# Kernel optimization log

Hardware: AMD Instinct MI355X
Metric: run time of the kernel (lower is better)

## Reference

```python
import jax, jax.numpy as jnp
import numpy as np

N_NODES = 100000
N_EDGES = 1600000
IN_DIM = 128
OUT_DIM = 64
SLOPE = 0.2


def setup_inputs() -> dict:
    key = jax.random.key(0)
    k1, k2, k3, k4 = jax.random.split(key, 4)
    h = jax.random.normal(k1, (N_NODES, IN_DIM), dtype=jnp.float32)
    W = jax.random.normal(k2, (OUT_DIM, IN_DIM), dtype=jnp.float32) * (1.0 / np.sqrt(IN_DIM))
    src = jax.random.randint(k3, (N_EDGES,), 0, N_NODES, dtype=jnp.int64)
    dst = jax.random.randint(k4, (N_EDGES,), 0, N_NODES, dtype=jnp.int64)
    return {"h": h, "W": W, "src": src, "dst": dst}


def reference(h, W, src, dst):
    n = h.shape[0]
    z = h @ W.T                                   # [N, out_dim]
    z_src = z[src]                                # [E, out_dim]
    z_dst = z[dst]                                # [E, out_dim]
    e = jax.nn.leaky_relu(jnp.sum(z_src * z_dst, axis=1), negative_slope=SLOPE)  # [E]
    # segment softmax over incoming edges of each destination node
    m = jax.ops.segment_max(e, dst, num_segments=n)        # [N], -inf for isolated nodes
    ex = jnp.exp(e - m[dst])                                # [E]
    denom = jax.ops.segment_sum(ex, dst, num_segments=n)    # [N]
    alpha = ex / denom[dst]                                 # [E]
    agg = jax.ops.segment_sum(alpha[:, None] * z_src, dst, num_segments=n)  # [N, out_dim]
    return jax.nn.elu(agg)
```

## Files before the change

### kernel.cpp

```cpp
#include <hip/hip_runtime.h>
#include <math.h>

#define SLOPE 0.2f
#define LOG2E 1.4426950408889634f

__global__ __launch_bounds__(256) void gemm_hist_kernel(const float* __restrict__ h,
                                                        const float* __restrict__ W,
                                                        float* __restrict__ z,
                                                        const int* __restrict__ dst,
                                                        int* __restrict__ cnt,
                                                        int* __restrict__ rank,
                                                        int n, int ne) {
    int ei = blockIdx.x * 256 + threadIdx.x;
    int base = ei * 4;
    if (base + 3 < ne) {
        int4 d = *(const int4*)(dst + base);
        int4 r;
        r.x = atomicAdd(&cnt[d.x], 1);
        r.y = atomicAdd(&cnt[d.y], 1);
        r.z = atomicAdd(&cnt[d.z], 1);
        r.w = atomicAdd(&cnt[d.w], 1);
        *(int4*)(rank + base) = r;
    } else if (base < ne) {
        for (int rr = base; rr < ne; rr++) rank[rr] = atomicAdd(&cnt[dst[rr]], 1);
    }

    __shared__ float ws[128][68];
    int t = threadIdx.x;
    const float4* __restrict__ W4 = reinterpret_cast<const float4*>(W);
#pragma unroll
    for (int j = 0; j < 8; j++) {
        int idx = t + j * 256;
        float4 w = W4[idx];
        int o = idx >> 5;
        int k = (idx & 31) << 2;
        ws[k + 0][o] = w.x; ws[k + 1][o] = w.y;
        ws[k + 2][o] = w.z; ws[k + 3][o] = w.w;
    }
    __syncthreads();

    int nb = blockIdx.x * 64;
    int ng = t >> 4, og = t & 15;
    int n0 = nb + ng * 4;
    if (n0 >= n) return;
    const float* __restrict__ hp = h + (size_t)n0 * 128;

    float acc[4][4] = {};
#pragma unroll 4
    for (int k = 0; k < 128; k += 4) {
        float4 hv[4], wv[4];
#pragma unroll
        for (int i = 0; i < 4; i++) hv[i] = *(const float4*)(hp + i * 128 + k);
#pragma unroll
        for (int kk = 0; kk < 4; kk++) wv[kk] = *(const float4*)&ws[k + kk][og * 4];
#pragma unroll
        for (int i = 0; i < 4; i++) {
            acc[i][0] += hv[i].x * wv[0].x + hv[i].y * wv[1].x + hv[i].z * wv[2].x + hv[i].w * wv[3].x;
            acc[i][1] += hv[i].x * wv[0].y + hv[i].y * wv[1].y + hv[i].z * wv[2].y + hv[i].w * wv[3].y;
            acc[i][2] += hv[i].x * wv[0].z + hv[i].y * wv[1].z + hv[i].z * wv[2].z + hv[i].w * wv[3].z;
            acc[i][3] += hv[i].x * wv[0].w + hv[i].y * wv[1].w + hv[i].z * wv[2].w + hv[i].w * wv[3].w;
        }
    }
#pragma unroll
    for (int i = 0; i < 4; i++) {
        *(float4*)&z[(size_t)(n0 + i) * 64 + og * 4] =
            make_float4(acc[i][0], acc[i][1], acc[i][2], acc[i][3]);
    }
}

__global__ __launch_bounds__(256) void scan1(const int* __restrict__ cnt,
                                             int* __restrict__ starts,
                                             int* __restrict__ bsums, int n) {
    __shared__ int ls[256];
    int tbase = blockIdx.x * 4096 + threadIdx.x * 16;
    int v[16];
    int s = 0;
#pragma unroll
    for (int k = 0; k < 16; k++) {
        int idx = tbase + k;
        int c = idx < n ? cnt[idx] : 0;
        v[k] = c; s += c;
    }
    ls[threadIdx.x] = s;
    __syncthreads();
    for (int off = 1; off < 256; off <<= 1) {
        int t = threadIdx.x >= off ? ls[threadIdx.x - off] : 0;
        __syncthreads();
        ls[threadIdx.x] += t;
        __syncthreads();
    }
    int run = ls[threadIdx.x] - s;
    if (threadIdx.x == 255) bsums[blockIdx.x] = ls[255];
#pragma unroll
    for (int k = 0; k < 16; k++) {
        int idx = tbase + k;
        if (idx < n) starts[idx] = run;
        run += v[k];
    }
}

__global__ void scan2(int* __restrict__ bsums, int nb, int* __restrict__ starts,
                      int n, int ne) {
    if (threadIdx.x == 0) {
        int run = 0;
        for (int b = 0; b < nb; b++) { int t = bsums[b]; bsums[b] = run; run += t; }
        starts[n] = ne;
    }
}

__global__ __launch_bounds__(256) void scan3(int* __restrict__ starts,
                                             const int* __restrict__ bsums, int n) {
    int i = blockIdx.x * 256 + threadIdx.x;
    if (i < n) starts[i] += bsums[i >> 12];
}

__global__ __launch_bounds__(256) void scatter4_kernel(const int* __restrict__ src,
                                                       const int* __restrict__ dst,
                                                       const int* __restrict__ starts,
                                                       const int* __restrict__ rank,
                                                       int* __restrict__ csr_src, int ne) {
    int i = blockIdx.x * 256 + threadIdx.x;
    int base = i * 4;
    if (base + 3 < ne) {
        int4 s = *(const int4*)(src + base);
        int4 d = *(const int4*)(dst + base);
        int4 r = *(const int4*)(rank + base);
        csr_src[starts[d.x] + r.x] = s.x;
        csr_src[starts[d.y] + r.y] = s.y;
        csr_src[starts[d.z] + r.z] = s.z;
        csr_src[starts[d.w] + r.w] = s.w;
    } else {
        for (int r = base; r < ne; r++)
            csr_src[starts[dst[r]] + rank[r]] = src[r];
    }
}

__global__ __launch_bounds__(256) void fused_node(const float4* __restrict__ z4,
                                                  const int* __restrict__ starts,
                                                  const int* __restrict__ csr_src,
                                                  float4* __restrict__ out4, int n) {
    int node = blockIdx.x * 4 + (threadIdx.x >> 6);
    if (node >= n) return;
    int lane = threadIdx.x & 63;
    int g = lane >> 4;
    int q = lane & 15;
    int rs = starts[node], re = starts[node + 1];
    float4 zd = z4[(size_t)node * 16 + q];

    float m2 = -1e30f, denom = 0.f;
    float4 acc = make_float4(0.f, 0.f, 0.f, 0.f);

    for (int c = rs; c < re; c += 64) {
        int j = c + lane;
        int sv = j < re ? csr_src[j] : 0;
        int cn = min(64, re - c);
        int idx = g;
        bool val = idx < cn;
        int s = __shfl(sv, val ? idx : 0);
        float4 v = z4[(size_t)s * 16 + q];
        for (int k = 0; k < cn; k += 4) {
            int idx_n = k + 4 + g;
            bool val_n = idx_n < cn;
            int s_n = __shfl(sv, val_n ? idx_n : 0);
            float4 vn = z4[(size_t)s_n * 16 + q];
            float p = v.x * zd.x + v.y * zd.y + v.z * zd.z + v.w * zd.w;
#pragma unroll
            for (int msk = 1; msk < 16; msk <<= 1) p += __shfl_xor(p, msk);
            float e = p > 0.f ? p : SLOPE * p;
            float e2 = e * LOG2E;
            e2 = val ? e2 : -2e30f;
            if (__any(e2 > m2)) {
                float mnew = fmaxf(m2, e2);
                float sc = exp2f(m2 - mnew);
                float ex = exp2f(e2 - mnew);
                denom = fmaf(denom, sc, ex);
                acc.x = fmaf(acc.x, sc, ex * v.x);
                acc.y = fmaf(acc.y, sc, ex * v.y);
                acc.z = fmaf(acc.z, sc, ex * v.z);
                acc.w = fmaf(acc.w, sc, ex * v.w);
                m2 = mnew;
            } else {
                float ex = exp2f(e2 - m2);
                denom += ex;
                acc.x = fmaf(ex, v.x, acc.x);
                acc.y = fmaf(ex, v.y, acc.y);
                acc.z = fmaf(ex, v.z, acc.z);
                acc.w = fmaf(ex, v.w, acc.w);
            }
            v = vn; val = val_n;
        }
    }
#pragma unroll
    for (int msk = 16; msk < 64; msk <<= 1) {
        float mo  = __shfl_xor(m2, msk);
        float dno = __shfl_xor(denom, msk);
        float ax = __shfl_xor(acc.x, msk);
        float ay = __shfl_xor(acc.y, msk);
        float az = __shfl_xor(acc.z, msk);
        float aw = __shfl_xor(acc.w, msk);
        float mnew = fmaxf(m2, mo);
        float ss = exp2f(m2 - mnew), so = exp2f(mo - mnew);
        denom = fmaf(denom, ss, dno * so);
        acc.x = fmaf(acc.x, ss, ax * so);
        acc.y = fmaf(acc.y, ss, ay * so);
        acc.z = fmaf(acc.z, ss, az * so);
        acc.w = fmaf(acc.w, ss, aw * so);
        m2 = mnew;
    }
    if (lane < 16) {
        float inv = denom > 0.f ? 1.f / denom : 0.f;
        float4 r; float x;
        x = acc.x * inv; r.x = x > 0.f ? x : __expf(x) - 1.f;
        x = acc.y * inv; r.y = x > 0.f ? x : __expf(x) - 1.f;
        x = acc.z * inv; r.z = x > 0.f ? x : __expf(x) - 1.f;
        x = acc.w * inv; r.w = x > 0.f ? x : __expf(x) - 1.f;
        out4[(size_t)node * 16 + q] = r;
    }
}

extern "C" void kernel_launch(void* const* d_in, const int* in_sizes, int n_in,
                              void* d_out, int out_size, void* d_ws, size_t ws_size,
                              hipStream_t stream) {
    const float* h   = (const float*)d_in[0];
    const float* W   = (const float*)d_in[1];
    const int*   src = (const int*)d_in[2];
    const int*   dst = (const int*)d_in[3];
    int n  = in_sizes[0] / 128;
    int ne = in_sizes[2];

    float* z       = (float*)d_ws;
    int*   starts  = (int*)(z + (size_t)n * 64);
    int*   cnt     = starts + (n + 1);
    int*   rank    = cnt + n;
    int*   csr_src = rank + ne;
    int*   bsums   = csr_src + ne;

    int nb_gemm = (n + 63) / 64;
    int nt4 = (ne + 3) / 4;
    int nb_scan = (n + 4095) / 4096;

    hipMemsetAsync(cnt, 0, (size_t)n * sizeof(int), stream);
    gemm_hist_kernel<<<nb_gemm, 256, 0, stream>>>(h, W, z, dst, cnt, rank, n, ne);
    scan1<<<nb_scan, 256, 0, stream>>>(cnt, starts, bsums, n);
    scan2<<<1, 64, 0, stream>>>(bsums, nb_scan, starts, n, ne);
    scan3<<<(n + 255) / 256, 256, 0, stream>>>(starts, bsums, n);
    scatter4_kernel<<<(nt4 + 255) / 256, 256, 0, stream>>>(src, dst, starts, rank,
                                                           csr_src, ne);
    fused_node<<<(n + 3) / 4, 256, 0, stream>>>((const float4*)z, starts, csr_src,
                                                (float4*)d_out, n);
}
```

Before: 211.7 us.

## Split GEMM output channels across two blocks with swizzled LDS and higher occupancy

Each 64-node tile of the fused GEMM+histogram kernel is now handled by two blocks, each computing 32 of the 64 output channels with a 2x4 per-thread register tile. The histogram part processes 2 edges per thread instead of 4, matching the doubled grid. Shared W storage is halved and stored with an XOR swizzle to avoid LDS bank conflicts, and launch bounds request 8 blocks per CU. The aim is more parallelism and occupancy in exchange for reading each h row twice and loading W twice.

```diff
diff --git a/kernel.cpp b/kernel.cpp
--- a/kernel.cpp
+++ b/kernel.cpp
@@ -4,57 +4,60 @@
 #define SLOPE 0.2f
 #define LOG2E 1.4426950408889634f
 
-__global__ __launch_bounds__(256) void gemm_hist_kernel(const float* __restrict__ h,
-                                                        const float* __restrict__ W,
-                                                        float* __restrict__ z,
-                                                        const int* __restrict__ dst,
-                                                        int* __restrict__ cnt,
-                                                        int* __restrict__ rank,
-                                                        int n, int ne) {
+__global__ __launch_bounds__(256, 8) void gemm_hist_kernel(const float* __restrict__ h,
+                                                           const float* __restrict__ W,
+                                                           float* __restrict__ z,
+                                                           const int* __restrict__ dst,
+                                                           int* __restrict__ cnt,
+                                                           int* __restrict__ rank,
+                                                           int n, int ne) {
     int ei = blockIdx.x * 256 + threadIdx.x;
-    int base = ei * 4;
-    if (base + 3 < ne) {
-        int4 d = *(const int4*)(dst + base);
-        int4 r;
+    int base = ei * 2;
+    if (base + 1 < ne) {
+        int2 d = *(const int2*)(dst + base);
+        int2 r;
         r.x = atomicAdd(&cnt[d.x], 1);
         r.y = atomicAdd(&cnt[d.y], 1);
-        r.z = atomicAdd(&cnt[d.z], 1);
-        r.w = atomicAdd(&cnt[d.w], 1);
-        *(int4*)(rank + base) = r;
+        *(int2*)(rank + base) = r;
     } else if (base < ne) {
-        for (int rr = base; rr < ne; rr++) rank[rr] = atomicAdd(&cnt[dst[rr]], 1);
-    }
-
-    __shared__ float ws[128][68];
+        rank[base] = atomicAdd(&cnt[dst[base]], 1);
+    }
+
+    __shared__ float ws[128][36];
     int t = threadIdx.x;
+    int nblk = blockIdx.x >> 1;
+    int ch0  = (blockIdx.x & 1) << 5;
     const float4* __restrict__ W4 = reinterpret_cast<const float4*>(W);
 #pragma unroll
-    for (int j = 0; j < 8; j++) {
+    for (int j = 0; j < 4; j++) {
         int idx = t + j * 256;
-        float4 w = W4[idx];
-        int o = idx >> 5;
-        int k = (idx & 31) << 2;
-        ws[k + 0][o] = w.x; ws[k + 1][o] = w.y;
-        ws[k + 2][o] = w.z; ws[k + 3][o] = w.w;
+        int o  = idx >> 5;
+        int kq = idx & 31;
+        float4 w = W4[(size_t)(ch0 + o) * 32 + kq];
+        int k = kq << 2;
+        int col = o ^ ((kq & 7) << 2);
+        ws[k + 0][col] = w.x; ws[k + 1][col] = w.y;
+        ws[k + 2][col] = w.z; ws[k + 3][col] = w.w;
     }
     __syncthreads();
 
-    int nb = blockIdx.x * 64;
-    int ng = t >> 4, og = t & 15;
-    int n0 = nb + ng * 4;
+    int ng = t >> 3, og = t & 7;
+    int n0 = nblk * 64 + ng * 2;
     if (n0 >= n) return;
     const float* __restrict__ hp = h + (size_t)n0 * 128;
 
-    float acc[4][4] = {};
+    float acc[2][4] = {};
 #pragma unroll 4
     for (int k = 0; k < 128; k += 4) {
-        float4 hv[4], wv[4];
-#pragma unroll
-        for (int i = 0; i < 4; i++) hv[i] = *(const float4*)(hp + i * 128 + k);
-#pragma unroll
-        for (int kk = 0; kk < 4; kk++) wv[kk] = *(const float4*)&ws[k + kk][og * 4];
-#pragma unroll
-        for (int i = 0; i < 4; i++) {
+        int m = (k >> 2) & 7;
+        int colb = (og ^ m) << 2;
+        float4 hv[2], wv[4];
+#pragma unroll
+        for (int i = 0; i < 2; i++) hv[i] = *(const float4*)(hp + i * 128 + k);
+#pragma unroll
+        for (int kk = 0; kk < 4; kk++) wv[kk] = *(const float4*)&ws[k + kk][colb];
+#pragma unroll
+        for (int i = 0; i < 2; i++) {
             acc[i][0] += hv[i].x * wv[0].x + hv[i].y * wv[1].x + hv[i].z * wv[2].x + hv[i].w * wv[3].x;
             acc[i][1] += hv[i].x * wv[0].y + hv[i].y * wv[1].y + hv[i].z * wv[2].y + hv[i].w * wv[3].y;
             acc[i][2] += hv[i].x * wv[0].z + hv[i].y * wv[1].z + hv[i].z * wv[2].z + hv[i].w * wv[3].z;
@@ -62,8 +65,8 @@
         }
     }
 #pragma unroll
-    for (int i = 0; i < 4; i++) {
-        *(float4*)&z[(size_t)(n0 + i) * 64 + og * 4] =
+    for (int i = 0; i < 2; i++) {
+        *(float4*)&z[(size_t)(n0 + i) * 64 + ch0 + og * 4] =
             make_float4(acc[i][0], acc[i][1], acc[i][2], acc[i][3]);
     }
 }
@@ -235,7 +238,7 @@
     int*   csr_src = rank + ne;
     int*   bsums   = csr_src + ne;
 
-    int nb_gemm = (n + 63) / 64;
+    int nb_gemm = ((n + 63) / 64) * 2;
     int nt4 = (ne + 3) / 4;
     int nb_scan = (n + 4095) / 4096;
 
```

Result: faster. 205.7 us (-2.9%).
